# Performance work log

Measured on AMD Instinct MI355X. Metric: run time of the kernel, lower is better.

Reference implementation:

```python
import jax, jax.numpy as jnp
import numpy as np

B = 4
N_SAMPLES = 32768
N_EVENTS = 32
N_HARMONICS = 16
SAMPLES_PER_FRAME = 256
N_FRAMES = N_SAMPLES // SAMPLES_PER_FRAME  # 128
SAMPLERATE = 22050
NYQ = SAMPLERATE // 2
MIN_F = 20.0 / NYQ
MAX_F = 4000.0 / NYQ
RES_BASE = 0.8
N_ROOMS = 8
LOG_SQRT_2PI = 0.5 * np.log(2.0 * np.pi).astype(np.float32)


def max_norm(x):
    return x / (jnp.max(jnp.abs(x), axis=-1, keepdims=True) + 1e-8)


def window(means, stds, n, mn, mx, eps=1e-8):
    # means/stds: [B, E, 1]; Normal pdf evaluated on linspace(0,1,n), max-normalized
    mu = mn + means * (mx - mn)
    sigma = eps + stds
    rng = jnp.linspace(0.0, 1.0, n, dtype=jnp.float32)[None, None, :]
    logp = -0.5 * ((rng - mu) / sigma) ** 2 - jnp.log(sigma) - LOG_SQRT_2PI
    return max_norm(jnp.exp(logp))


def interp_linear(x, out_size):
    # F.interpolate(mode='linear', align_corners=False) along last axis
    in_size = x.shape[-1]
    coords = (jnp.arange(out_size, dtype=jnp.float32) + 0.5) * (in_size / out_size) - 0.5
    coords = jnp.clip(coords, 0.0, in_size - 1.0)
    lo = jnp.floor(coords).astype(jnp.int32)
    hi = jnp.minimum(lo + 1, in_size - 1)
    w = (coords - lo.astype(jnp.float32))
    return x[..., lo] * (1.0 - w) + x[..., hi] * w


def fft_convolve(a, b):
    # zero-padded linear convolution via FFT, truncated to original length
    n = a.shape[-1]
    pa = jnp.pad(a, [(0, 0)] * (a.ndim - 1) + [(0, n)])
    pb = jnp.pad(b, [(0, 0)] * (b.ndim - 1) + [(0, n)])
    out = jnp.fft.irfft(jnp.fft.rfft(pa) * jnp.fft.rfft(pb), n=2 * n)
    return out[..., :n]


def setup_inputs():
    key = jax.random.key(0)
    k1, k2, k3, k4, k5 = jax.random.split(key, 5)
    return {
        'event_params': jax.random.uniform(k1, (B, N_EVENTS, N_HARMONICS + 6), dtype=jnp.float32),
        'mx_raw': jax.random.normal(k2, (B,), dtype=jnp.float32),
        'room_logits': jax.random.normal(k3, (B, N_ROOMS), dtype=jnp.float32),
        'noise': jax.random.uniform(k4, (1, 1, N_SAMPLES), dtype=jnp.float32, minval=-1.0, maxval=1.0),
        'impulse_responses': jax.random.normal(k5, (N_ROOMS, N_SAMPLES), dtype=jnp.float32) * 0.01,
    }


def reference(event_params, mx_raw, room_logits, noise, impulse_responses):
    b = event_params.shape[0]
    ep = event_params  # [B, E, 22], already in [0,1] (post-activation)
    freq_means = ep[:, :, 0:1] ** 2
    freq_stds = ep[:, :, 1:2] * 0.1
    time_means = ep[:, :, 2:3]
    time_stds = ep[:, :, 3:4] * 0.1
    f0 = ep[:, :, 4:5] ** 2
    amps = ep[:, :, 5:6] ** 2
    res = ep[:, :, 6:] * (1.0 - RES_BASE) + RES_BASE  # [B, E, H]
    mx = jax.nn.sigmoid(mx_raw).reshape(b, 1, 1)
    rooms = jax.nn.softmax(room_logits, axis=-1)

    # --- BandLimitedNoise ---
    nfft = N_SAMPLES // 2 + 1
    win = window(freq_means, freq_stds, nfft, MIN_F, MAX_F)  # [B, E, nfft]
    noise_spec = jnp.fft.rfft(noise, norm='ortho')            # [1, 1, nfft]
    bl_noise = jnp.fft.irfft(noise_spec * win, n=N_SAMPLES, norm='ortho')  # [B, E, N]

    # --- impulse (time) windows ---
    events = window(time_means, time_stds, N_SAMPLES, 0.0, 1.0)  # [B, E, N]

    # --- Resonance ---
    factors = jnp.arange(1, N_HARMONICS + 1, dtype=jnp.float32)
    f0s = MIN_F + (MAX_F - MIN_F) * f0                 # [B, E, 1]
    freqs = f0s * factors                               # [B, E, H]
    freqs = jnp.where(freqs >= 1.0, 0.0, freqs)
    freqs_fr = jnp.broadcast_to(freqs[..., None], freqs.shape + (N_FRAMES,))
    freqs_s = interp_linear(freqs_fr, N_SAMPLES)        # [B, E, H, N]
    res_fr = jnp.cumprod(jnp.broadcast_to(res[..., None], res.shape + (N_FRAMES,)), axis=-1)
    res_s = interp_linear(res_fr, N_SAMPLES)            # [B, E, H, N]
    resonances = jnp.sum(res_s * jnp.sin(jnp.cumsum(freqs_s * (2.0 * np.pi), axis=-1)), axis=2)  # [B, E, N]

    # --- locate events + resonance convolution (noise_coeff = 1) ---
    located = bl_noise * events * amps
    located = fft_convolve(located, resonances) + located
    located = jnp.sum(located, axis=1, keepdims=True)   # [B, 1, N]

    # --- reverb: rooms-weighted impulse response, dry/wet mix ---
    dry = located
    imp = jnp.einsum('br,rn->bn', rooms, impulse_responses)[:, None, :]
    wet = fft_convolve(located, imp)
    return dry * (1.0 - mx) + wet * mx
```

## Files before the change

kernel.cpp:

```cpp
#include <hip/hip_runtime.h>
#include <math.h>

#define NSAMP 32768
#define NPAD  65536
#define NCH   128
#define NCHAIN 2048
#define TWO_PI 6.2831853071795864f

__device__ __forceinline__ float2 cxmul(float2 a, float2 b){
    return make_float2(a.x*b.x - a.y*b.y, a.x*b.y + a.y*b.x);
}

template<int DIR>
__device__ __forceinline__ void fft4v(float2* v, int i0, int i1, int i2, int i3){
    float2 a=v[i0], b=v[i1], c=v[i2], d=v[i3];
    float2 t0 = make_float2(a.x+c.x, a.y+c.y);
    float2 t1 = make_float2(a.x-c.x, a.y-c.y);
    float2 t2 = make_float2(b.x+d.x, b.y+d.y);
    float2 t3 = make_float2(b.x-d.x, b.y-d.y);
    v[i0] = make_float2(t0.x+t2.x, t0.y+t2.y);
    v[i2] = make_float2(t0.x-t2.x, t0.y-t2.y);
    if (DIR < 0) {
        v[i1] = make_float2(t1.x + t3.y, t1.y - t3.x);
        v[i3] = make_float2(t1.x - t3.y, t1.y + t3.x);
    } else {
        v[i1] = make_float2(t1.x - t3.y, t1.y + t3.x);
        v[i3] = make_float2(t1.x + t3.y, t1.y - t3.x);
    }
}

template<int DIR>
__device__ __forceinline__ void twm(float2& v, float c, float s){
    float sy = (DIR<0) ? -s : s;
    v = cxmul(v, make_float2(c, sy));
}

template<int DIR>
__device__ __forceinline__ void fft16r(float2* v){
    const float C1=0.92387953251128674f, S1=0.38268343236508978f, H=0.70710678118654752f;
    fft4v<DIR>(v,0,4,8,12);
    fft4v<DIR>(v,1,5,9,13);
    fft4v<DIR>(v,2,6,10,14);
    fft4v<DIR>(v,3,7,11,15);
    twm<DIR>(v[5],  C1, S1);
    twm<DIR>(v[6],  H,  H);
    twm<DIR>(v[7],  S1, C1);
    twm<DIR>(v[9],  H,  H);
    twm<DIR>(v[10], 0.0f, 1.0f);
    twm<DIR>(v[11], -H, H);
    twm<DIR>(v[13], S1, C1);
    twm<DIR>(v[14], -H, H);
    twm<DIR>(v[15], -C1, -S1);
    fft4v<DIR>(v,0,1,2,3);
    fft4v<DIR>(v,4,5,6,7);
    fft4v<DIR>(v,8,9,10,11);
    fft4v<DIR>(v,12,13,14,15);
}

template<int DIR>
__device__ __forceinline__ void fft8r(float2* v){
    const float H=0.70710678118654752f;
    #pragma unroll
    for (int n1=0;n1<4;n1++){
        float2 t=v[n1], u=v[n1+4];
        v[n1]   = make_float2(t.x+u.x, t.y+u.y);
        v[n1+4] = make_float2(t.x-u.x, t.y-u.y);
    }
    twm<DIR>(v[5], H, H);
    twm<DIR>(v[6], 0.0f, 1.0f);
    twm<DIR>(v[7], -H, H);
    fft4v<DIR>(v,0,1,2,3);
    fft4v<DIR>(v,4,5,6,7);
}

__device__ __forceinline__ int slot16(int r){ return ((r&3)<<2)|(r>>2); }
__device__ __forceinline__ int slot8(int r){ return ((r&1)<<2)|(r>>1); }
__device__ __forceinline__ int lpad(int l){ return l + (l>>4); }

template<int R, int DIR>
__global__ __launch_bounds__(256) void mfk_fft(const float2* __restrict__ src,
                                               float2* __restrict__ dst,
                                               int Ns, int T)
{
    int j = blockIdx.x*256 + threadIdx.x;
    if (j >= T) return;
    size_t aoff = (size_t)blockIdx.y * (size_t)T * (size_t)R;
    const float2* x = src + aoff;
    float2* y = dst + aoff;
    float2 v[R];
    #pragma unroll
    for (int r=0;r<R;r++) v[r] = x[j + r*T];
    int jm = j & (Ns-1);
    if (jm) {
        float base = (DIR<0 ? -TWO_PI : TWO_PI) * ((float)jm / (float)(Ns*R));
        #pragma unroll
        for (int r=1;r<R;r++){
            float s,c; __sincosf(base*(float)r, &s, &c);
            v[r] = cxmul(v[r], make_float2(c,s));
        }
    }
    if (R==16) fft16r<DIR>(v); else fft8r<DIR>(v);
    int idxD = (j & ~(Ns-1))*R + jm;
    float2* yo = y + idxD;
    #pragma unroll
    for (int r=0;r<R;r++){
        int slot = (R==16) ? slot16(r) : slot8(r);
        yo[r*Ns] = v[slot];
    }
}

__global__ __launch_bounds__(256) void mfk_noise_fft1(const float* __restrict__ noise,
                                                      float2* __restrict__ dst)
{
    int j = blockIdx.x*256 + threadIdx.x;
    float2 v[16];
    #pragma unroll
    for (int r=0;r<16;r++) v[r] = make_float2(noise[j + r*2048], 0.0f);
    fft16r<-1>(v);
    float2* yo = dst + j*16;
    #pragma unroll
    for (int r=0;r<16;r++) yo[r] = v[slot16(r)];
}

__global__ __launch_bounds__(256) void mfk_specwin_fft1(const float2* __restrict__ nspec,
        const float* __restrict__ chP, float2* __restrict__ dst, int g0)
{
    int j = blockIdx.x*256 + threadIdx.x;
    int p = blockIdx.y;
    int c0 = g0 + 2*p;
    const float* A = chP + c0*8;
    const float* B = chP + (c0+1)*8;
    float a0=A[0], a1=A[1], a2=A[2], b0=B[0], b1=B[1], b2=B[2];
    float2 v[16];
    #pragma unroll
    for (int r=0;r<16;r++){
        int k = j + r*2048;
        int kw = (k <= 16384) ? k : (32768 - k);
        float rg = (float)kw * (1.0f/16384.0f);
        float t0 = (rg - a0)*a1;
        float w0 = expf(-0.5f*t0*t0)*a2;
        float t1 = (rg - b0)*b1;
        float w1 = expf(-0.5f*t1*t1)*b2;
        float2 N = nspec[k];
        v[r] = make_float2(N.x*w0 - N.y*w1, N.y*w0 + N.x*w1);
    }
    fft16r<1>(v);
    float2* yo = dst + (size_t)p*NSAMP + j*16;
    #pragma unroll
    for (int r=0;r<16;r++) yo[r] = v[slot16(r)];
}

__global__ __launch_bounds__(256) void mfk_unpack_fftL(const float2* __restrict__ src,
        const float* __restrict__ chP, float* __restrict__ locraw, int g0)
{
    const int Ns = 4096, T = 4096;
    int j = blockIdx.x*256 + threadIdx.x;
    int p = blockIdx.y;
    const float2* x = src + (size_t)p*NSAMP;
    float2 v[8];
    #pragma unroll
    for (int r=0;r<8;r++) v[r] = x[j + r*T];
    int jm = j & (Ns-1);
    if (jm) {
        float base = TWO_PI * ((float)jm / (float)(Ns*8));
        #pragma unroll
        for (int r=1;r<8;r++){
            float s,c; __sincosf(base*(float)r, &s, &c);
            v[r] = cxmul(v[r], make_float2(c,s));
        }
    }
    fft8r<1>(v);
    int lc0 = 2*p;
    const float* C0 = chP + (g0+lc0)*8;
    const float* C1 = chP + (g0+lc0+1)*8;
    float c03=C0[3], c04=C0[4], c05=C0[5], c06=C0[6];
    float c13=C1[3], c14=C1[4], c15=C1[5], c16=C1[6];
    #pragma unroll
    for (int r=0;r<8;r++){
        int n = j + r*Ns;
        float2 val = v[slot8(r)];
        float rg = (float)((double)n * (1.0/32767.0));
        float tt0 = (rg - c03)*c04;
        float ew0 = expf(-0.5f*tt0*tt0)*c05;
        float tt1 = (rg - c13)*c14;
        float ew1 = expf(-0.5f*tt1*tt1)*c15;
        locraw[(size_t)lc0*NSAMP + n]     = val.x*(1.0f/32768.0f)*ew0*c06;
        locraw[(size_t)(lc0+1)*NSAMP + n] = val.y*(1.0f/32768.0f)*ew1*c16;
    }
}

template<int DIR>
__device__ __forceinline__ void fuse01_tail(float2 (&v)[16], float2* lds, int t, int p,
                                            float2* __restrict__ outB)
{
    fft16r<DIR>(v);
    int r2 = t>>4, w = t&15;
    #pragma unroll
    for (int r=0;r<16;r++) lds[lpad(256*r2 + 16*w + r)] = v[slot16(r)];
    __syncthreads();
    #pragma unroll
    for (int q=0;q<16;q++) v[q] = lds[lpad(256*q + t)];
    int j2 = 256*p + t;
    int jm = t & 15;
    if (jm){
        float base = (DIR<0?-TWO_PI:TWO_PI) * ((float)jm * (1.0f/256.0f));
        #pragma unroll
        for (int r=1;r<16;r++){ float s,c; __sincosf(base*(float)r,&s,&c); v[r]=cxmul(v[r],make_float2(c,s)); }
    }
    fft16r<DIR>(v);
    float2* yo = outB + (j2>>4)*256 + (j2&15);
    #pragma unroll
    for (int r=0;r<16;r++) yo[16*r] = v[slot16(r)];
}

__global__ __launch_bounds__(256) void mfk_packZ_f01(const float* __restrict__ locraw,
        const float* __restrict__ reson, float2* __restrict__ dst)
{
    __shared__ float2 lds[4352];
    int t = threadIdx.x, p = blockIdx.x, lc = blockIdx.y;
    int j = 256*(t>>4) + 16*p + (t&15);
    const float* la = locraw + (size_t)lc*NSAMP;
    const float* ra = reson  + (size_t)lc*NSAMP;
    float2 v[16];
    #pragma unroll
    for (int r=0;r<8;r++){ int n = j + 4096*r; v[r] = make_float2(la[n], ra[n]); }
    #pragma unroll
    for (int r=8;r<16;r++) v[r] = make_float2(0.f,0.f);
    fuse01_tail<-1>(v, lds, t, p, dst + (size_t)lc*NPAD);
}

__global__ __launch_bounds__(256) void mfk_prod_f01(const float2* __restrict__ Z,
        float2* __restrict__ dst)
{
    __shared__ float2 lds[4352];
    int t = threadIdx.x, p = blockIdx.x, pr = blockIdx.y;
    const float2* z0 = Z + (size_t)(2*pr)*NPAD;
    const float2* z1 = z0 + NPAD;
    int j = 256*(t>>4) + 16*p + (t&15);
    float2 v[16];
    #pragma unroll
    for (int r=0;r<16;r++){
        int k = j + 4096*r;
        int km = (NPAD - k) & (NPAD-1);
        float2 a = z0[k], am = z0[km];
        float2 A0 = make_float2(0.5f*(a.x+am.x), 0.5f*(a.y-am.y));
        float2 R0 = make_float2(0.5f*(a.y+am.y), -0.5f*(a.x-am.x));
        float2 P0 = cxmul(A0,R0);
        float2 b = z1[k], bm = z1[km];
        float2 A1 = make_float2(0.5f*(b.x+bm.x), 0.5f*(b.y-bm.y));
        float2 R1 = make_float2(0.5f*(b.y+bm.y), -0.5f*(b.x-bm.x));
        float2 P1 = cxmul(A1,R1);
        const float s = 1.0f/65536.0f;
        v[r] = make_float2((P0.x - P1.y)*s, (P0.y + P1.x)*s);
    }
    fuse01_tail<1>(v, lds, t, p, dst + (size_t)pr*NPAD);
}

__global__ __launch_bounds__(256) void mfk_dry_f01(const float* __restrict__ located,
        const float* __restrict__ rmA, const float* __restrict__ IR, float2* __restrict__ dst)
{
    __shared__ float2 lds[4352];
    int t = threadIdx.x, p = blockIdx.x, b = blockIdx.y;
    int j = 256*(t>>4) + 16*p + (t&15);
    float rm[8];
    #pragma unroll
    for (int r=0;r<8;r++) rm[r] = rmA[b*8+r];
    float2 v[16];
    #pragma unroll
    for (int r=0;r<8;r++){
        int n = j + 4096*r;
        float iv = 0.f;
        #pragma unroll
        for (int q=0;q<8;q++) iv += rm[q]*IR[(size_t)q*NSAMP + n];
        v[r] = make_float2(located[(size_t)b*NSAMP + n], iv);
    }
    #pragma unroll
    for (int r=8;r<16;r++) v[r] = make_float2(0.f,0.f);
    fuse01_tail<-1>(v, lds, t, p, dst + (size_t)b*NPAD);
}

template<int DIR, int NSTORE>
__global__ __launch_bounds__(256) void mfk_f23(const float2* __restrict__ src,
                                               float2* __restrict__ dst)
{
    __shared__ float2 lds[4352];
    int t = threadIdx.x, p = blockIdx.x;
    size_t boff = (size_t)blockIdx.y * NPAD;
    int a = t>>4, w = t&15;
    int j = 256*a + 16*p + w;
    const float2* x = src + boff;
    float2 v[16];
    #pragma unroll
    for (int r=0;r<16;r++) v[r] = x[j + 4096*r];
    int jm = 16*p + w;
    if (jm){
        float base = (DIR<0?-TWO_PI:TWO_PI)*((float)jm*(1.0f/4096.0f));
        #pragma unroll
        for (int r=1;r<16;r++){ float s,c; __sincosf(base*(float)r,&s,&c); v[r]=cxmul(v[r],make_float2(c,s)); }
    }
    fft16r<DIR>(v);
    #pragma unroll
    for (int r=0;r<16;r++) lds[lpad(256*a + 16*r + w)] = v[slot16(r)];
    __syncthreads();
    #pragma unroll
    for (int q=0;q<16;q++) v[q] = lds[lpad(256*q + t)];
    {
        float base = (DIR<0?-TWO_PI:TWO_PI)*((float)j*(1.0f/65536.0f));
        #pragma unroll
        for (int r=1;r<16;r++){ float s,c; __sincosf(base*(float)r,&s,&c); v[r]=cxmul(v[r],make_float2(c,s)); }
    }
    fft16r<DIR>(v);
    float2* yo = dst + boff + j;
    #pragma unroll
    for (int r=0;r<NSTORE;r++) yo[4096*r] = v[slot16(r)];
}

__global__ __launch_bounds__(256) void mfk_f23_final(const float2* __restrict__ src,
        const float* __restrict__ located, const float* __restrict__ mxA,
        float* __restrict__ out)
{
    __shared__ float2 lds[4352];
    int t = threadIdx.x, p = blockIdx.x;
    size_t boff = (size_t)blockIdx.y * NPAD;
    int a = t>>4, w = t&15;
    int j = 256*a + 16*p + w;
    const float2* x = src + boff;
    float2 v[16];
    #pragma unroll
    for (int r=0;r<16;r++) v[r] = x[j + 4096*r];
    int jm = 16*p + w;
    if (jm){
        float base = TWO_PI*((float)jm*(1.0f/4096.0f));
        #pragma unroll
        for (int r=1;r<16;r++){ float s,c; __sincosf(base*(float)r,&s,&c); v[r]=cxmul(v[r],make_float2(c,s)); }
    }
    fft16r<1>(v);
    #pragma unroll
    for (int r=0;r<16;r++) lds[lpad(256*a + 16*r + w)] = v[slot16(r)];
    __syncthreads();
    #pragma unroll
    for (int q=0;q<16;q++) v[q] = lds[lpad(256*q + t)];
    {
        float base = TWO_PI*((float)j*(1.0f/65536.0f));
        #pragma unroll
        for (int r=1;r<16;r++){ float s,c; __sincosf(base*(float)r,&s,&c); v[r]=cxmul(v[r],make_float2(c,s)); }
    }
    fft16r<1>(v);
    int b0 = 2*blockIdx.y, b1 = b0+1;
    float mx0 = mxA[b0], mx1 = mxA[b1];
    #pragma unroll
    for (int r=0;r<8;r++){
        int ts = j + 4096*r;
        float2 val = v[slot16(r)];
        out[(size_t)b0*NSAMP+ts] = located[(size_t)b0*NSAMP+ts]*(1.f-mx0) + val.x*mx0;
        out[(size_t)b1*NSAMP+ts] = located[(size_t)b1*NSAMP+ts]*(1.f-mx1) + val.y*mx1;
    }
}

__global__ __launch_bounds__(256) void mfk_setup(const float* __restrict__ EP, const float* __restrict__ MXR,
        const float* __restrict__ RL, float* __restrict__ chP,
        unsigned* __restrict__ chQ, float* __restrict__ cum,
        float* __restrict__ mxA, float* __restrict__ rmA)
{
    int q = blockIdx.x*256 + threadIdx.x;
    if (q >= NCHAIN) return;
    int c = q >> 4, h = q & 15;
    const float* P = EP + c*22;
    const float MINF = (float)(20.0/11025.0);
    const float DRF  = (float)(4000.0/11025.0 - 20.0/11025.0);
    const float LSQ  = (float)0.9189385332046727;
    float f0m = __fmul_rn(P[4], P[4]);
    float f0s = __fadd_rn(MINF, __fmul_rn(f0m, DRF));
    float fr  = __fmul_rn(f0s, (float)(h+1));
    if (fr >= 1.0f) fr = 0.0f;
    double fd = (double)fr * 4294967296.0;
    chQ[q] = (unsigned)(unsigned long long)(fd + 0.5);
    float rs = __fadd_rn(__fmul_rn(P[6+h], 0.2f), 0.8f);
    float cp = rs;
    float* crow = cum + (size_t)q*128;
    for (int j=0;j<128;j++){ crow[j] = cp; cp = __fmul_rn(cp, rs); }
    if (h == 0) {
        float fm  = __fmul_rn(P[0],P[0]);
        float fmu = __fadd_rn(MINF, __fmul_rn(fm, DRF));
        float fsg = 1e-8f + P[1]*0.1f;
        float fsi = 1.0f/fsg;
        int i0 = (int)floorf(fmu*16384.0f + 0.5f);
        i0 = min(max(i0,0),16384);
        float rg = (float)i0 * (1.0f/16384.0f);
        float tt = (rg - fmu)*fsi;
        float Lc = logf(fsg) + LSQ;
        float sc = expf(-Lc) / (expf(-0.5f*tt*tt - Lc) + 1e-8f);
        float tmu = P[2];
        float tsg = 1e-8f + P[3]*0.1f;
        float tsi = 1.0f/tsg;
        int i1 = (int)floorf(tmu*32767.0f + 0.5f);
        i1 = min(max(i1,0),32767);
        float rg1 = (float)((double)i1 * (1.0/32767.0));
        float tt1 = (rg1 - tmu)*tsi;
        float Lc1 = logf(tsg) + LSQ;
        float sc1 = expf(-Lc1) / (expf(-0.5f*tt1*tt1 - Lc1) + 1e-8f);
        float amp = P[5]*P[5];
        float* o = chP + c*8;
        o[0]=fmu; o[1]=fsi; o[2]=sc; o[3]=tmu; o[4]=tsi; o[5]=sc1; o[6]=amp; o[7]=0.f;
    }
    if (q < 4) {
        int b = q;
        mxA[b] = 1.0f/(1.0f + expf(-MXR[b]));
        const float* rl = RL + b*8;
        float mx = rl[0];
        for (int r=1;r<8;r++) mx = fmaxf(mx, rl[r]);
        float sum=0.f;
        float e2[8];
        for (int r=0;r<8;r++){ e2[r]=expf(rl[r]-mx); sum+=e2[r]; }
        for (int r=0;r<8;r++) rmA[b*8+r] = e2[r]/sum;
    }
}

__global__ __launch_bounds__(256) void mfk_reson(const unsigned* __restrict__ chQ,
        const float* __restrict__ cum, float* __restrict__ reson, int g0)
{
    __shared__ float cp3[16][4];
    __shared__ unsigned qf[16];
    int j  = blockIdx.x;
    int lc = blockIdx.y;
    int cg = g0 + lc;
    int tid = threadIdx.x;
    int base = max(j-1, 0);
    if (tid < 16) {
        int q = cg*16 + tid;
        qf[tid] = chQ[q];
        const float* crow = cum + (size_t)q*128;
        cp3[tid][0] = crow[min(base+0,127)];
        cp3[tid][1] = crow[min(base+1,127)];
        cp3[tid][2] = crow[min(base+2,127)];
    }
    __syncthreads();
    int t = j*256 + tid;
    float co = ((float)t + 0.5f)*0.00390625f - 0.5f;
    co = fminf(fmaxf(co, 0.0f), 127.0f);
    int lo = (int)floorf(co);
    float w = co - (float)lo;
    int s0 = lo - base;
    int s1 = min(lo+1, 127) - base;
    unsigned T1 = (unsigned)(t+1);
    float acc = (t == 0) ? 1.0f : 0.0f;
    #pragma unroll
    for (int hh=0; hh<16; hh++){
        float e0 = cp3[hh][s0], e1 = cp3[hh][s1];
        float env = e0 + (e1-e0)*w;
        unsigned bits = qf[hh] * T1;
        float m = (float)bits * 2.3283064365386963e-10f;
        float sv;
        asm("v_sin_f32 %0, %1" : "=v"(sv) : "v"(m));
        acc = fmaf(env, sv, acc);
    }
    reson[(size_t)lc*NSAMP + t] = acc;
}

__global__ __launch_bounds__(256) void mfk_accum(const float2* __restrict__ U,
        float* __restrict__ located, int g0, int eStart, int eCount, int bBase)
{
    int t = blockIdx.x*256 + threadIdx.x;
    int b = bBase + blockIdx.y;
    float sum = 0.f;
    for (int ei=0; ei<eCount; ei++){
        int lc = b*32 + eStart + ei - g0;
        float2 u = U[(size_t)(lc>>1)*NPAD + t];
        sum += (lc & 1) ? u.y : u.x;
    }
    located[(size_t)b*NSAMP + t] += sum;
}

extern "C" void kernel_launch(void* const* d_in, const int* in_sizes, int n_in,
                              void* d_out, int out_size, void* d_ws, size_t ws_size,
                              hipStream_t stream)
{
    (void)in_sizes; (void)n_in; (void)out_size;
    const float* EP   = (const float*)d_in[0];
    const float* MXR  = (const float*)d_in[1];
    const float* RL   = (const float*)d_in[2];
    const float* NOISE= (const float*)d_in[3];
    const float* IR   = (const float*)d_in[4];
    float* out = (float*)d_out;
    char* w = (char*)d_ws;

    auto need = [](long long g)->long long {
        return 2LL*g*NPAD*8 + 2LL*g*NSAMP*4 + (long long)NSAMP*8
             + 1LL*NCHAIN*128*4 + (128LL*8 + NCHAIN + 4 + 32 + 4LL*NSAMP)*4 + 16384;
    };
    int G = 128;
    while (G > 4 && need(G) > (long long)ws_size) G >>= 1;

    size_t off = 0;
    auto alloc = [&](size_t bytes)->char* {
        char* p = w + off; off += (bytes + 255) & ~(size_t)255; return p;
    };
    float2*   arA    = (float2*)alloc((size_t)G*NPAD*8);
    float2*   arB    = (float2*)alloc((size_t)G*NPAD*8);
    float*    locraw = (float*) alloc((size_t)G*NSAMP*4);
    float*    reson  = (float*) alloc((size_t)G*NSAMP*4);
    float2*   nspec  = (float2*)alloc((size_t)NSAMP*8);
    float*    cum    = (float*) alloc((size_t)NCHAIN*128*4);
    float*    chP    = (float*) alloc(128*8*4);
    unsigned* chQ    = (unsigned*)alloc(NCHAIN*4);
    float*    mxA    = (float*) alloc(4*4);
    float*    rmA    = (float*) alloc(32*4);
    float*    located= (float*) alloc(4*NSAMP*4);

    (void)hipMemsetAsync(located, 0, 4*NSAMP*4, stream);
    mfk_setup<<<dim3(8),256,0,stream>>>(EP,MXR,RL,chP,chQ,cum,mxA,rmA);

    mfk_noise_fft1<<<dim3(8),256,0,stream>>>(NOISE, arB);
    mfk_fft<16,-1><<<dim3(8,1),256,0,stream>>>(arB, arA, 16,   2048);
    mfk_fft<16,-1><<<dim3(8,1),256,0,stream>>>(arA, arB, 256,  2048);
    mfk_fft<8, -1><<<dim3(16,1),256,0,stream>>>(arB, nspec, 4096, 4096);

    for (int g0 = 0; g0 < NCH; g0 += G){
        int P = G/2;
        mfk_specwin_fft1<<<dim3(8,P),256,0,stream>>>(nspec, chP, arA, g0);
        mfk_fft<16,1><<<dim3(8,P),256,0,stream>>>(arA, arB, 16,  2048);
        mfk_fft<16,1><<<dim3(8,P),256,0,stream>>>(arB, arA, 256, 2048);
        mfk_unpack_fftL<<<dim3(16,P),256,0,stream>>>(arA, chP, locraw, g0);
        mfk_reson<<<dim3(128,G),256,0,stream>>>(chQ, cum, reson, g0);
        mfk_packZ_f01<<<dim3(16,G),256,0,stream>>>(locraw, reson, arA);
        mfk_f23<-1,16><<<dim3(16,G),256,0,stream>>>(arA, arB);
        mfk_prod_f01<<<dim3(16,P),256,0,stream>>>(arB, arA);
        mfk_f23<1,8><<<dim3(16,P),256,0,stream>>>(arA, arB);
        int bBase, bCnt, eStart, eCount;
        if (G >= 32){ bBase = g0/32; bCnt = G/32; eStart = 0; eCount = 32; }
        else        { bBase = g0/32; bCnt = 1; eStart = g0 % 32; eCount = G; }
        mfk_accum<<<dim3(128,bCnt),256,0,stream>>>(arB, located, g0, eStart, eCount, bBase);
    }

    mfk_dry_f01<<<dim3(16,4),256,0,stream>>>(located, rmA, IR, arA);
    mfk_f23<-1,16><<<dim3(16,4),256,0,stream>>>(arA, arB);
    mfk_prod_f01<<<dim3(16,2),256,0,stream>>>(arB, arA);
    mfk_f23_final<<<dim3(16,2),256,0,stream>>>(arA, located, mxA, out);
}
```

Baseline: 201.9 us.

## Fuse FFT stages through LDS and compute resonance inline in pack kernel

The 32768-point noise and spectral-window FFTs are regrouped from four single-radix passes into two kernels that run two radix stages each with an LDS transpose in between, which removes intermediate global round trips. The resonance synthesis and its cumulative-product table now run inside the pack/FFT kernel, so the separate reson buffer, the cum table and their kernel launches go away. Twiddles are built by complex multiplication from a single sincos instead of one sincos per element. The located memset is replaced by an overwrite-or-accumulate flag, and prod_f01 remaps its block index. Each pack block recomputes its 16x128 cumprod table serially and carries more per-thread work, and products of twiddles may lose a little accuracy.

```diff
diff --git a/kernel.cpp b/kernel.cpp
--- a/kernel.cpp
+++ b/kernel.cpp
@@ -4,8 +4,9 @@
 #define NSAMP 32768
 #define NPAD  65536
 #define NCH   128
-#define NCHAIN 2048
 #define TWO_PI 6.2831853071795864f
+#define MINF ((float)(20.0/11025.0))
+#define DRF  ((float)(4000.0/11025.0 - 20.0/11025.0))
 
 __device__ __forceinline__ float2 cxmul(float2 a, float2 b){
     return make_float2(a.x*b.x - a.y*b.y, a.x*b.y + a.y*b.x);
@@ -77,64 +78,62 @@
 __device__ __forceinline__ int slot8(int r){ return ((r&1)<<2)|(r>>1); }
 __device__ __forceinline__ int lpad(int l){ return l + (l>>4); }
 
-template<int R, int DIR>
-__global__ __launch_bounds__(256) void mfk_fft(const float2* __restrict__ src,
-                                               float2* __restrict__ dst,
-                                               int Ns, int T)
-{
-    int j = blockIdx.x*256 + threadIdx.x;
-    if (j >= T) return;
-    size_t aoff = (size_t)blockIdx.y * (size_t)T * (size_t)R;
-    const float2* x = src + aoff;
-    float2* y = dst + aoff;
-    float2 v[R];
-    #pragma unroll
-    for (int r=0;r<R;r++) v[r] = x[j + r*T];
-    int jm = j & (Ns-1);
-    if (jm) {
-        float base = (DIR<0 ? -TWO_PI : TWO_PI) * ((float)jm / (float)(Ns*R));
-        #pragma unroll
-        for (int r=1;r<R;r++){
-            float s,c; __sincosf(base*(float)r, &s, &c);
-            v[r] = cxmul(v[r], make_float2(c,s));
-        }
-    }
-    if (R==16) fft16r<DIR>(v); else fft8r<DIR>(v);
-    int idxD = (j & ~(Ns-1))*R + jm;
-    float2* yo = y + idxD;
-    #pragma unroll
-    for (int r=0;r<R;r++){
-        int slot = (R==16) ? slot16(r) : slot8(r);
-        yo[r*Ns] = v[slot];
-    }
-}
-
-__global__ __launch_bounds__(256) void mfk_noise_fft1(const float* __restrict__ noise,
-                                                      float2* __restrict__ dst)
-{
-    int j = blockIdx.x*256 + threadIdx.x;
-    float2 v[16];
-    #pragma unroll
-    for (int r=0;r<16;r++) v[r] = make_float2(noise[j + r*2048], 0.0f);
-    fft16r<-1>(v);
-    float2* yo = dst + j*16;
-    #pragma unroll
-    for (int r=0;r<16;r++) yo[r] = v[slot16(r)];
-}
-
-__global__ __launch_bounds__(256) void mfk_specwin_fft1(const float2* __restrict__ nspec,
+template<int R>
+__device__ __forceinline__ void twiddle(float2* v, float ang1){
+    float s,c; __sincosf(ang1,&s,&c);
+    float2 w[R];
+    w[1] = make_float2(c,s);
+    #pragma unroll
+    for (int r=2;r<R;r++) w[r] = cxmul(w[r>>1], w[r-(r>>1)]);
+    #pragma unroll
+    for (int r=1;r<R;r++) v[r] = cxmul(v[r], w[r]);
+}
+
+template<int DIR>
+__device__ __forceinline__ void n1_tail(float2 (&v)[16], float2* lds, int t, int p,
+                                        float2* __restrict__ out)
+{
+    fft16r<DIR>(v);
+    #pragma unroll
+    for (int r=0;r<16;r++) lds[lpad(256*(t>>4) + 16*(t&15) + r)] = v[slot16(r)];
+    __syncthreads();
+    #pragma unroll
+    for (int q=0;q<16;q++) v[q] = lds[lpad(256*q + t)];
+    int jm = t & 15;
+    if (jm) twiddle<16>(v, (DIR<0?-TWO_PI:TWO_PI)*(float)jm*(1.0f/256.0f));
+    fft16r<DIR>(v);
+    int j2 = 256*p + t;
+    float2* yo = out + (j2>>4)*256 + (j2&15);
+    #pragma unroll
+    for (int r=0;r<16;r++) yo[16*r] = v[slot16(r)];
+}
+
+__global__ __launch_bounds__(256) void mfk_n1_noise(const float* __restrict__ noise,
+                                                    float2* __restrict__ dst)
+{
+    __shared__ float2 lds[4352];
+    int t = threadIdx.x, p = blockIdx.x;
+    int j = 128*(t>>4) + 16*p + (t&15);
+    float2 v[16];
+    #pragma unroll
+    for (int r=0;r<16;r++) v[r] = make_float2(noise[j + 2048*r], 0.0f);
+    n1_tail<-1>(v, lds, t, p, dst);
+}
+
+__global__ __launch_bounds__(256) void mfk_n1_specwin(const float2* __restrict__ nspec,
         const float* __restrict__ chP, float2* __restrict__ dst, int g0)
 {
-    int j = blockIdx.x*256 + threadIdx.x;
-    int p = blockIdx.y;
-    int c0 = g0 + 2*p;
+    __shared__ float2 lds[4352];
+    int t = threadIdx.x, p = blockIdx.x, pr = blockIdx.y;
+    int c0 = g0 + 2*pr;
     const float* A = chP + c0*8;
     const float* B = chP + (c0+1)*8;
     float a0=A[0], a1=A[1], a2=A[2], b0=B[0], b1=B[1], b2=B[2];
+    int j = 128*(t>>4) + 16*p + (t&15);
     float2 v[16];
     #pragma unroll
     for (int r=0;r<16;r++){
-        int k = j + r*2048;
+        int k = j + 2048*r;
         int kw = (k <= 16384) ? k : (32768 - k);
         float rg = (float)kw * (1.0f/16384.0f);
         float t0 = (rg - a0)*a1;
@@ -144,96 +143,138 @@
         float2 N = nspec[k];
         v[r] = make_float2(N.x*w0 - N.y*w1, N.y*w0 + N.x*w1);
     }
-    fft16r<1>(v);
-    float2* yo = dst + (size_t)p*NSAMP + j*16;
-    #pragma unroll
-    for (int r=0;r<16;r++) yo[r] = v[slot16(r)];
-}
-
-__global__ __launch_bounds__(256) void mfk_unpack_fftL(const float2* __restrict__ src,
+    n1_tail<1>(v, lds, t, p, dst + (size_t)pr*NSAMP);
+}
+
+template<int DIR>
+__device__ __forceinline__ void n2_stageC(const float2* __restrict__ x, float2* lds, int t, int p)
+{
+    float2 v[16];
+    int j2 = 256*(t>>5) + 32*p + (t&31);
+    #pragma unroll
+    for (int r=0;r<16;r++) v[r] = x[j2 + 2048*r];
+    int jm = 32*p + (t&31);
+    if (jm) twiddle<16>(v, (DIR<0?-TWO_PI:TWO_PI)*(float)jm*(1.0f/4096.0f));
+    fft16r<DIR>(v);
+    #pragma unroll
+    for (int r=0;r<16;r++) lds[lpad(256*r + t)] = v[slot16(r)];
+    __syncthreads();
+}
+
+template<int DIR>
+__device__ __forceinline__ int n2_stageD(float2* lds, int t, int p, int u, float2 (&w8)[8])
+{
+    int q = t + 256*u;
+    int j3 = ((q>>5)<<8) + 32*p + (q&31);
+    #pragma unroll
+    for (int r3=0;r3<8;r3++) w8[r3] = lds[lpad(256*(q>>5) + 32*r3 + (q&31))];
+    if (j3) twiddle<8>(w8, (DIR<0?-TWO_PI:TWO_PI)*(float)j3*(1.0f/32768.0f));
+    fft8r<DIR>(w8);
+    return j3;
+}
+
+__global__ __launch_bounds__(256) void mfk_n2_noise(const float2* __restrict__ src,
+                                                    float2* __restrict__ dst)
+{
+    __shared__ float2 lds[4352];
+    int t = threadIdx.x, p = blockIdx.x;
+    n2_stageC<-1>(src, lds, t, p);
+    #pragma unroll
+    for (int u=0;u<2;u++){
+        float2 w8[8];
+        int j3 = n2_stageD<-1>(lds, t, p, u, w8);
+        #pragma unroll
+        for (int r=0;r<8;r++) dst[j3 + 4096*r] = w8[slot8(r)];
+    }
+}
+
+__global__ __launch_bounds__(256) void mfk_n2_unpack(const float2* __restrict__ src,
         const float* __restrict__ chP, float* __restrict__ locraw, int g0)
 {
-    const int Ns = 4096, T = 4096;
-    int j = blockIdx.x*256 + threadIdx.x;
-    int p = blockIdx.y;
-    const float2* x = src + (size_t)p*NSAMP;
-    float2 v[8];
-    #pragma unroll
-    for (int r=0;r<8;r++) v[r] = x[j + r*T];
-    int jm = j & (Ns-1);
-    if (jm) {
-        float base = TWO_PI * ((float)jm / (float)(Ns*8));
-        #pragma unroll
-        for (int r=1;r<8;r++){
-            float s,c; __sincosf(base*(float)r, &s, &c);
-            v[r] = cxmul(v[r], make_float2(c,s));
-        }
-    }
-    fft8r<1>(v);
-    int lc0 = 2*p;
+    __shared__ float2 lds[4352];
+    int t = threadIdx.x, p = blockIdx.x, pr = blockIdx.y;
+    n2_stageC<1>(src + (size_t)pr*NSAMP, lds, t, p);
+    int lc0 = 2*pr;
     const float* C0 = chP + (g0+lc0)*8;
     const float* C1 = chP + (g0+lc0+1)*8;
     float c03=C0[3], c04=C0[4], c05=C0[5], c06=C0[6];
     float c13=C1[3], c14=C1[4], c15=C1[5], c16=C1[6];
     #pragma unroll
-    for (int r=0;r<8;r++){
-        int n = j + r*Ns;
-        float2 val = v[slot8(r)];
-        float rg = (float)((double)n * (1.0/32767.0));
-        float tt0 = (rg - c03)*c04;
-        float ew0 = expf(-0.5f*tt0*tt0)*c05;
-        float tt1 = (rg - c13)*c14;
-        float ew1 = expf(-0.5f*tt1*tt1)*c15;
-        locraw[(size_t)lc0*NSAMP + n]     = val.x*(1.0f/32768.0f)*ew0*c06;
-        locraw[(size_t)(lc0+1)*NSAMP + n] = val.y*(1.0f/32768.0f)*ew1*c16;
-    }
-}
-
-template<int DIR>
-__device__ __forceinline__ void fuse01_tail(float2 (&v)[16], float2* lds, int t, int p,
-                                            float2* __restrict__ outB)
-{
-    fft16r<DIR>(v);
-    int r2 = t>>4, w = t&15;
-    #pragma unroll
-    for (int r=0;r<16;r++) lds[lpad(256*r2 + 16*w + r)] = v[slot16(r)];
+    for (int u=0;u<2;u++){
+        float2 w8[8];
+        int j3 = n2_stageD<1>(lds, t, p, u, w8);
+        #pragma unroll
+        for (int r=0;r<8;r++){
+            int n = j3 + 4096*r;
+            float2 val = w8[slot8(r)];
+            float rg = (float)((double)n * (1.0/32767.0));
+            float tt0 = (rg - c03)*c04;
+            float ew0 = expf(-0.5f*tt0*tt0)*c05;
+            float tt1 = (rg - c13)*c14;
+            float ew1 = expf(-0.5f*tt1*tt1)*c15;
+            locraw[(size_t)lc0*NSAMP + n]     = val.x*(1.0f/32768.0f)*ew0*c06;
+            locraw[(size_t)(lc0+1)*NSAMP + n] = val.y*(1.0f/32768.0f)*ew1*c16;
+        }
+    }
+}
+
+__global__ __launch_bounds__(256) void mfk_packZres_f01(const float* __restrict__ locraw,
+        const float* __restrict__ EP, float2* __restrict__ dst, int g0)
+{
+    __shared__ float2 lds[4352];
+    __shared__ float cumS[16][128];
+    __shared__ unsigned qS[16];
+    int t = threadIdx.x, p = blockIdx.x, lc = blockIdx.y;
+    int cg = g0 + lc;
+    if (t < 16){
+        const float* P = EP + cg*22;
+        float f0m = __fmul_rn(P[4],P[4]);
+        float f0s = __fadd_rn(MINF, __fmul_rn(f0m, DRF));
+        float fr  = __fmul_rn(f0s, (float)(t+1));
+        if (fr >= 1.0f) fr = 0.0f;
+        qS[t] = (unsigned)(unsigned long long)((double)fr*4294967296.0 + 0.5);
+        float rs = __fadd_rn(__fmul_rn(P[6+t],0.2f),0.8f);
+        float cp = rs;
+        for (int jj=0;jj<128;jj++){ cumS[t][jj] = cp; cp = __fmul_rn(cp, rs); }
+    }
     __syncthreads();
-    #pragma unroll
-    for (int q=0;q<16;q++) v[q] = lds[lpad(256*q + t)];
-    int j2 = 256*p + t;
-    int jm = t & 15;
-    if (jm){
-        float base = (DIR<0?-TWO_PI:TWO_PI) * ((float)jm * (1.0f/256.0f));
-        #pragma unroll
-        for (int r=1;r<16;r++){ float s,c; __sincosf(base*(float)r,&s,&c); v[r]=cxmul(v[r],make_float2(c,s)); }
-    }
-    fft16r<DIR>(v);
-    float2* yo = outB + (j2>>4)*256 + (j2&15);
-    #pragma unroll
-    for (int r=0;r<16;r++) yo[16*r] = v[slot16(r)];
-}
-
-__global__ __launch_bounds__(256) void mfk_packZ_f01(const float* __restrict__ locraw,
-        const float* __restrict__ reson, float2* __restrict__ dst)
-{
-    __shared__ float2 lds[4352];
-    int t = threadIdx.x, p = blockIdx.x, lc = blockIdx.y;
     int j = 256*(t>>4) + 16*p + (t&15);
     const float* la = locraw + (size_t)lc*NSAMP;
-    const float* ra = reson  + (size_t)lc*NSAMP;
-    float2 v[16];
-    #pragma unroll
-    for (int r=0;r<8;r++){ int n = j + 4096*r; v[r] = make_float2(la[n], ra[n]); }
+    float2 v[16];
+    #pragma unroll
+    for (int r=0;r<8;r++){
+        int n = j + 4096*r;
+        float co = ((float)n + 0.5f)*0.00390625f - 0.5f;
+        co = fminf(fmaxf(co,0.0f),127.0f);
+        int lo = (int)co;
+        float wf = co - (float)lo;
+        int hi = min(lo+1,127);
+        unsigned T1 = (unsigned)(n+1);
+        float acc = (n==0) ? 1.0f : 0.0f;
+        #pragma unroll
+        for (int hh=0; hh<16; hh++){
+            float e0 = cumS[hh][lo], e1 = cumS[hh][hi];
+            float env = e0 + (e1-e0)*wf;
+            unsigned bits = qS[hh]*T1;
+            float m = (float)bits * 2.3283064365386963e-10f;
+            float sv; asm("v_sin_f32 %0, %1" : "=v"(sv) : "v"(m));
+            acc = fmaf(env, sv, acc);
+        }
+        v[r] = make_float2(la[n], acc);
+    }
     #pragma unroll
     for (int r=8;r<16;r++) v[r] = make_float2(0.f,0.f);
-    fuse01_tail<-1>(v, lds, t, p, dst + (size_t)lc*NPAD);
+    n1_tail<-1>(v, lds, t, p, dst + (size_t)lc*NPAD);
 }
 
 __global__ __launch_bounds__(256) void mfk_prod_f01(const float2* __restrict__ Z,
         float2* __restrict__ dst)
 {
     __shared__ float2 lds[4352];
-    int t = threadIdx.x, p = blockIdx.x, pr = blockIdx.y;
+    int t = threadIdx.x;
+    int px = blockIdx.x;
+    int p = (px < 8) ? px : 23 - px;
+    int pr = blockIdx.y;
     const float2* z0 = Z + (size_t)(2*pr)*NPAD;
     const float2* z1 = z0 + NPAD;
     int j = 256*(t>>4) + 16*p + (t&15);
@@ -253,7 +294,7 @@
         const float s = 1.0f/65536.0f;
         v[r] = make_float2((P0.x - P1.y)*s, (P0.y + P1.x)*s);
     }
-    fuse01_tail<1>(v, lds, t, p, dst + (size_t)pr*NPAD);
+    n1_tail<1>(v, lds, t, p, dst + (size_t)pr*NPAD);
 }
 
 __global__ __launch_bounds__(256) void mfk_dry_f01(const float* __restrict__ located,
@@ -276,7 +317,7 @@
     }
     #pragma unroll
     for (int r=8;r<16;r++) v[r] = make_float2(0.f,0.f);
-    fuse01_tail<-1>(v, lds, t, p, dst + (size_t)b*NPAD);
+    n1_tail<-1>(v, lds, t, p, dst + (size_t)b*NPAD);
 }
 
 template<int DIR, int NSTORE>
@@ -293,22 +334,14 @@
     #pragma unroll
     for (int r=0;r<16;r++) v[r] = x[j + 4096*r];
     int jm = 16*p + w;
-    if (jm){
-        float base = (DIR<0?-TWO_PI:TWO_PI)*((float)jm*(1.0f/4096.0f));
-        #pragma unroll
-        for (int r=1;r<16;r++){ float s,c; __sincosf(base*(float)r,&s,&c); v[r]=cxmul(v[r],make_float2(c,s)); }
-    }
+    if (jm) twiddle<16>(v, (DIR<0?-TWO_PI:TWO_PI)*(float)jm*(1.0f/4096.0f));
     fft16r<DIR>(v);
     #pragma unroll
     for (int r=0;r<16;r++) lds[lpad(256*a + 16*r + w)] = v[slot16(r)];
     __syncthreads();
     #pragma unroll
     for (int q=0;q<16;q++) v[q] = lds[lpad(256*q + t)];
-    {
-        float base = (DIR<0?-TWO_PI:TWO_PI)*((float)j*(1.0f/65536.0f));
-        #pragma unroll
-        for (int r=1;r<16;r++){ float s,c; __sincosf(base*(float)r,&s,&c); v[r]=cxmul(v[r],make_float2(c,s)); }
-    }
+    if (j) twiddle<16>(v, (DIR<0?-TWO_PI:TWO_PI)*(float)j*(1.0f/65536.0f));
     fft16r<DIR>(v);
     float2* yo = dst + boff + j;
     #pragma unroll
@@ -329,22 +362,14 @@
     #pragma unroll
     for (int r=0;r<16;r++) v[r] = x[j + 4096*r];
     int jm = 16*p + w;
-    if (jm){
-        float base = TWO_PI*((float)jm*(1.0f/4096.0f));
-        #pragma unroll
-        for (int r=1;r<16;r++){ float s,c; __sincosf(base*(float)r,&s,&c); v[r]=cxmul(v[r],make_float2(c,s)); }
-    }
+    if (jm) twiddle<16>(v, TWO_PI*(float)jm*(1.0f/4096.0f));
     fft16r<1>(v);
     #pragma unroll
     for (int r=0;r<16;r++) lds[lpad(256*a + 16*r + w)] = v[slot16(r)];
     __syncthreads();
     #pragma unroll
     for (int q=0;q<16;q++) v[q] = lds[lpad(256*q + t)];
-    {
-        float base = TWO_PI*((float)j*(1.0f/65536.0f));
-        #pragma unroll
-        for (int r=1;r<16;r++){ float s,c; __sincosf(base*(float)r,&s,&c); v[r]=cxmul(v[r],make_float2(c,s)); }
-    }
+    if (j) twiddle<16>(v, TWO_PI*(float)j*(1.0f/65536.0f));
     fft16r<1>(v);
     int b0 = 2*blockIdx.y, b1 = b0+1;
     float mx0 = mxA[b0], mx1 = mxA[b1];
@@ -357,29 +382,14 @@
     }
 }
 
-__global__ __launch_bounds__(256) void mfk_setup(const float* __restrict__ EP, const float* __restrict__ MXR,
-        const float* __restrict__ RL, float* __restrict__ chP,
-        unsigned* __restrict__ chQ, float* __restrict__ cum,
-        float* __restrict__ mxA, float* __restrict__ rmA)
-{
-    int q = blockIdx.x*256 + threadIdx.x;
-    if (q >= NCHAIN) return;
-    int c = q >> 4, h = q & 15;
-    const float* P = EP + c*22;
-    const float MINF = (float)(20.0/11025.0);
-    const float DRF  = (float)(4000.0/11025.0 - 20.0/11025.0);
-    const float LSQ  = (float)0.9189385332046727;
-    float f0m = __fmul_rn(P[4], P[4]);
-    float f0s = __fadd_rn(MINF, __fmul_rn(f0m, DRF));
-    float fr  = __fmul_rn(f0s, (float)(h+1));
-    if (fr >= 1.0f) fr = 0.0f;
-    double fd = (double)fr * 4294967296.0;
-    chQ[q] = (unsigned)(unsigned long long)(fd + 0.5);
-    float rs = __fadd_rn(__fmul_rn(P[6+h], 0.2f), 0.8f);
-    float cp = rs;
-    float* crow = cum + (size_t)q*128;
-    for (int j=0;j<128;j++){ crow[j] = cp; cp = __fmul_rn(cp, rs); }
-    if (h == 0) {
+__global__ __launch_bounds__(256) void mfk_setup(const float* __restrict__ EP,
+        const float* __restrict__ MXR, const float* __restrict__ RL,
+        float* __restrict__ chP, float* __restrict__ mxA, float* __restrict__ rmA)
+{
+    int t = threadIdx.x;
+    const float LSQ = (float)0.9189385332046727;
+    if (t < NCH){
+        const float* P = EP + t*22;
         float fm  = __fmul_rn(P[0],P[0]);
         float fmu = __fadd_rn(MINF, __fmul_rn(fm, DRF));
         float fsg = 1e-8f + P[1]*0.1f;
@@ -400,11 +410,11 @@
         float Lc1 = logf(tsg) + LSQ;
         float sc1 = expf(-Lc1) / (expf(-0.5f*tt1*tt1 - Lc1) + 1e-8f);
         float amp = P[5]*P[5];
-        float* o = chP + c*8;
+        float* o = chP + t*8;
         o[0]=fmu; o[1]=fsi; o[2]=sc; o[3]=tmu; o[4]=tsi; o[5]=sc1; o[6]=amp; o[7]=0.f;
     }
-    if (q < 4) {
-        int b = q;
+    if (t < 4){
+        int b = t;
         mxA[b] = 1.0f/(1.0f + expf(-MXR[b]));
         const float* rl = RL + b*8;
         float mx = rl[0];
@@ -416,49 +426,8 @@
     }
 }
 
-__global__ __launch_bounds__(256) void mfk_reson(const unsigned* __restrict__ chQ,
-        const float* __restrict__ cum, float* __restrict__ reson, int g0)
-{
-    __shared__ float cp3[16][4];
-    __shared__ unsigned qf[16];
-    int j  = blockIdx.x;
-    int lc = blockIdx.y;
-    int cg = g0 + lc;
-    int tid = threadIdx.x;
-    int base = max(j-1, 0);
-    if (tid < 16) {
-        int q = cg*16 + tid;
-        qf[tid] = chQ[q];
-        const float* crow = cum + (size_t)q*128;
-        cp3[tid][0] = crow[min(base+0,127)];
-        cp3[tid][1] = crow[min(base+1,127)];
-        cp3[tid][2] = crow[min(base+2,127)];
-    }
-    __syncthreads();
-    int t = j*256 + tid;
-    float co = ((float)t + 0.5f)*0.00390625f - 0.5f;
-    co = fminf(fmaxf(co, 0.0f), 127.0f);
-    int lo = (int)floorf(co);
-    float w = co - (float)lo;
-    int s0 = lo - base;
-    int s1 = min(lo+1, 127) - base;
-    unsigned T1 = (unsigned)(t+1);
-    float acc = (t == 0) ? 1.0f : 0.0f;
-    #pragma unroll
-    for (int hh=0; hh<16; hh++){
-        float e0 = cp3[hh][s0], e1 = cp3[hh][s1];
-        float env = e0 + (e1-e0)*w;
-        unsigned bits = qf[hh] * T1;
-        float m = (float)bits * 2.3283064365386963e-10f;
-        float sv;
-        asm("v_sin_f32 %0, %1" : "=v"(sv) : "v"(m));
-        acc = fmaf(env, sv, acc);
-    }
-    reson[(size_t)lc*NSAMP + t] = acc;
-}
-
 __global__ __launch_bounds__(256) void mfk_accum(const float2* __restrict__ U,
-        float* __restrict__ located, int g0, int eStart, int eCount, int bBase)
+        float* __restrict__ located, int g0, int eStart, int eCount, int bBase, int addTo)
 {
     int t = blockIdx.x*256 + threadIdx.x;
     int b = bBase + blockIdx.y;
@@ -468,7 +437,9 @@
         float2 u = U[(size_t)(lc>>1)*NPAD + t];
         sum += (lc & 1) ? u.y : u.x;
     }
-    located[(size_t)b*NSAMP + t] += sum;
+    size_t idx = (size_t)b*NSAMP + t;
+    float base0 = addTo ? located[idx] : 0.0f;
+    located[idx] = base0 + sum;
 }
 
 extern "C" void kernel_launch(void* const* d_in, const int* in_sizes, int n_in,
@@ -485,8 +456,8 @@
     char* w = (char*)d_ws;
 
     auto need = [](long long g)->long long {
-        return 2LL*g*NPAD*8 + 2LL*g*NSAMP*4 + (long long)NSAMP*8
-             + 1LL*NCHAIN*128*4 + (128LL*8 + NCHAIN + 4 + 32 + 4LL*NSAMP)*4 + 16384;
+        return 2LL*g*NPAD*8 + 1LL*g*NSAMP*4 + (long long)NSAMP*8
+             + (128LL*8 + 4 + 32 + 4LL*NSAMP)*4 + 16384;
     };
     int G = 128;
     while (G > 4 && need(G) > (long long)ws_size) G >>= 1;
@@ -498,38 +469,30 @@
     float2*   arA    = (float2*)alloc((size_t)G*NPAD*8);
     float2*   arB    = (float2*)alloc((size_t)G*NPAD*8);
     float*    locraw = (float*) alloc((size_t)G*NSAMP*4);
-    float*    reson  = (float*) alloc((size_t)G*NSAMP*4);
     float2*   nspec  = (float2*)alloc((size_t)NSAMP*8);
-    float*    cum    = (float*) alloc((size_t)NCHAIN*128*4);
     float*    chP    = (float*) alloc(128*8*4);
-    unsigned* chQ    = (unsigned*)alloc(NCHAIN*4);
     float*    mxA    = (float*) alloc(4*4);
     float*    rmA    = (float*) alloc(32*4);
     float*    located= (float*) alloc(4*NSAMP*4);
 
-    (void)hipMemsetAsync(located, 0, 4*NSAMP*4, stream);
-    mfk_setup<<<dim3(8),256,0,stream>>>(EP,MXR,RL,chP,chQ,cum,mxA,rmA);
-
-    mfk_noise_fft1<<<dim3(8),256,0,stream>>>(NOISE, arB);
-    mfk_fft<16,-1><<<dim3(8,1),256,0,stream>>>(arB, arA, 16,   2048);
-    mfk_fft<16,-1><<<dim3(8,1),256,0,stream>>>(arA, arB, 256,  2048);
-    mfk_fft<8, -1><<<dim3(16,1),256,0,stream>>>(arB, nspec, 4096, 4096);
+    mfk_setup<<<dim3(1),256,0,stream>>>(EP,MXR,RL,chP,mxA,rmA);
+
+    mfk_n1_noise<<<dim3(8),256,0,stream>>>(NOISE, arB);
+    mfk_n2_noise<<<dim3(8),256,0,stream>>>(arB, nspec);
 
     for (int g0 = 0; g0 < NCH; g0 += G){
         int P = G/2;
-        mfk_specwin_fft1<<<dim3(8,P),256,0,stream>>>(nspec, chP, arA, g0);
-        mfk_fft<16,1><<<dim3(8,P),256,0,stream>>>(arA, arB, 16,  2048);
-        mfk_fft<16,1><<<dim3(8,P),256,0,stream>>>(arB, arA, 256, 2048);
-        mfk_unpack_fftL<<<dim3(16,P),256,0,stream>>>(arA, chP, locraw, g0);
-        mfk_reson<<<dim3(128,G),256,0,stream>>>(chQ, cum, reson, g0);
-        mfk_packZ_f01<<<dim3(16,G),256,0,stream>>>(locraw, reson, arA);
+        mfk_n1_specwin<<<dim3(8,P),256,0,stream>>>(nspec, chP, arA, g0);
+        mfk_n2_unpack<<<dim3(8,P),256,0,stream>>>(arA, chP, locraw, g0);
+        mfk_packZres_f01<<<dim3(16,G),256,0,stream>>>(locraw, EP, arA, g0);
         mfk_f23<-1,16><<<dim3(16,G),256,0,stream>>>(arA, arB);
         mfk_prod_f01<<<dim3(16,P),256,0,stream>>>(arB, arA);
         mfk_f23<1,8><<<dim3(16,P),256,0,stream>>>(arA, arB);
         int bBase, bCnt, eStart, eCount;
         if (G >= 32){ bBase = g0/32; bCnt = G/32; eStart = 0; eCount = 32; }
         else        { bBase = g0/32; bCnt = 1; eStart = g0 % 32; eCount = G; }
-        mfk_accum<<<dim3(128,bCnt),256,0,stream>>>(arB, located, g0, eStart, eCount, bBase);
+        int addTo = (eStart != 0);
+        mfk_accum<<<dim3(128,bCnt),256,0,stream>>>(arB, located, g0, eStart, eCount, bBase, addTo);
     }
 
     mfk_dry_f01<<<dim3(16,4),256,0,stream>>>(located, rmA, IR, arA);
```

Result: faster. 195.1 us (-3.4%).
